# Kernel tuning notes

Measured on AMD Instinct MI355X. Metric: run time of the kernel, lower is better.

The kernel has to match this reference:

```python
import jax, jax.numpy as jnp
import numpy as np


def setup_inputs() -> dict:
    key = jax.random.key(0)
    ks = jax.random.split(key, 8)
    B, N, C = 4, 2048, 1024
    H, hd, lr, R = 16, 64, 20, 200  # R = low_rank * rank_multi
    s = lambda k, shape, fan: jax.random.normal(k, shape, jnp.float32) / np.sqrt(fan)
    return {
        'x': jax.random.normal(ks[0], (B, N, C), jnp.float32),
        'qk_w': s(ks[1], (2 * C, C), C),
        'proj_w': s(ks[2], (C, C), C),
        'proj_b': jnp.zeros((C,), jnp.float32),
        'we': s(ks[3], (H, R, lr), R),
        'wr': s(ks[4], (H, R, lr), R),
        'cw_w': s(ks[5], (hd, 2 * lr), 2 * lr),
        'cw_b': jnp.zeros((hd,), jnp.float32),
    }


def _l2norm(v, eps=1e-12):
    # matches F.normalize(p=2, dim=-1): x / max(||x||, eps)
    n = jnp.sqrt(jnp.sum(v * v, axis=-1, keepdims=True))
    return v / jnp.maximum(n, eps)


def reference(x, qk_w, proj_w, proj_b, we, wr, cw_w, cw_b):
    B, N, C = x.shape
    H, R, lr = we.shape  # heads, subsample len, low_rank
    hd = C // H
    # qk projection -> q,k: [B,H,N,hd]
    qk = (x @ qk_w.T).reshape(B, N, 2, H, hd).transpose(2, 0, 3, 1, 4)
    q, k = qk[0], qk[1]
    # gen_weights: subsample N positions (embed_len > low_rank*rank_multi branch)
    idx = np.linspace(0, N - 1, R).astype(np.int64)  # static, trunc like torch
    xh = x.transpose(0, 2, 1).reshape(B, H, hd, N)[:, :, :, idx]  # [B,H,hd,R]
    we_b = jnp.einsum('bhdr,hre->bhde', xh, we)  # [B,H,hd,lr]
    wr_b = jnp.einsum('bhdr,hre->bhde', xh, wr)
    # feature map + low-rank scores
    q = _l2norm(q)
    k = _l2norm(k)
    escore = jnp.einsum('bhnd,bhde->bhne', q, we_b)  # [B,H,N,lr]
    rscore = jnp.einsum('bhnd,bhde->bhne', k, wr_b)
    score = jnp.concatenate([escore, rscore], axis=-1)  # [B,H,N,2lr]
    attn = score @ cw_w.T + cw_b  # [B,H,N,hd]
    attn = attn.transpose(0, 2, 1, 3).reshape(B, N, C)
    out = attn @ proj_w.T + proj_b  # dropout is identity at eval
    return out
```

## Files before the change

### kernel.cpp

```cpp
#include <hip/hip_runtime.h>
#include <hip/hip_bf16.h>

constexpr int B_  = 4;
constexpr int N_  = 2048;
constexpr int C_  = 1024;
constexpr int H_  = 16;
constexpr int HD  = 64;
constexpr int LR  = 20;
constexpr int RS  = 200;
constexpr int RP  = 224;

typedef __attribute__((ext_vector_type(8))) short bf16x8;
typedef __attribute__((ext_vector_type(4))) float f32x4;

__device__ __forceinline__ float b2f_raw(unsigned short u) {
    union { unsigned int i; float f; } v;
    v.i = ((unsigned int)u) << 16;
    return v.f;
}
__device__ __forceinline__ unsigned short f2b(float f) {
    __hip_bfloat16 h = __float2bfloat16(f);
    return *(unsigned short*)&h;
}
template <bool BF>
__device__ __forceinline__ float ldg(const void* p, size_t i) {
    if constexpr (BF) return b2f_raw(((const unsigned short*)p)[i]);
    else              return ((const float*)p)[i];
}

__device__ __forceinline__ void async_load16(const unsigned short* g, unsigned short* l) {
    __builtin_amdgcn_global_load_lds(
        (const __attribute__((address_space(1))) unsigned int*)(const void*)g,
        (__attribute__((address_space(3))) unsigned int*)(void*)l,
        16, 0, 0);
}

__global__ __launch_bounds__(256)
void detect_kernel(const unsigned int* __restrict__ x, int* __restrict__ flag) {
    const int t = threadIdx.x;
    int cnt = 0;
    for (int i = t; i < 1024; i += 256) {
        const unsigned int w = x[i];
        const unsigned int e = (w >> 7) & 0xFFu;
        cnt += (e >= 103u && e <= 140u) ? 1 : 0;
    }
    __shared__ int s[256];
    s[t] = cnt;
    __syncthreads();
    for (int off = 128; off > 0; off >>= 1) {
        if (t < off) s[t] += s[t + off];
        __syncthreads();
    }
    if (t == 0) *flag = (s[0] > 512) ? 1 : 0;
}

struct CvtArgs {
    const void* src[5];
    unsigned short* dst[5];
    int size[5];
};

template <bool BF>
__device__ void wec_body(const void* __restrict__ we_raw,
                         const void* __restrict__ wr_raw,
                         const void* __restrict__ cw_raw,
                         unsigned short* __restrict__ wect,
                         unsigned short* __restrict__ wrct) {
    const int o = blockIdx.x * 256 + threadIdx.x;
    if (o >= H_ * HD * RP) return;
    const int r    = o % RP;
    const int dout = (o / RP) % HD;
    const int h    = o / (RP * HD);
    float sq = 0.f, sk = 0.f;
    if (r < RS) {
        #pragma unroll
        for (int e = 0; e < LR; ++e) {
            const float cq = ldg<BF>(cw_raw, dout * 2 * LR + e);
            const float ck = ldg<BF>(cw_raw, dout * 2 * LR + LR + e);
            sq += ldg<BF>(we_raw, ((size_t)h * RS + r) * LR + e) * cq;
            sk += ldg<BF>(wr_raw, ((size_t)h * RS + r) * LR + e) * ck;
        }
    }
    wect[o] = f2b(sq);
    wrct[o] = f2b(sk);
}

template <bool BF>
__device__ void gather_body(const void* __restrict__ x_raw,
                            unsigned short* __restrict__ xh) {
    const int bh = blockIdx.x;
    if (bh >= B_ * H_) return;
    const int b = bh >> 4;
    const int h = bh & 15;
    for (int o = threadIdx.x; o < HD * RP; o += 256) {
        const int din = o & 63;
        const int r   = o >> 6;
        unsigned short v = 0;
        if (r < RS) {
            const int ir = (r * (N_ - 1)) / (RS - 1);
            const size_t idx = ((size_t)b * N_ + ir) * C_ + h * HD + din;
            if constexpr (BF) v = ((const unsigned short*)x_raw)[idx];
            else              v = f2b(((const float*)x_raw)[idx]);
        }
        xh[(size_t)bh * HD * RP + (size_t)din * RP + r] = v;
    }
}

__global__ __launch_bounds__(256)
void fused_prep_kernel(const int* __restrict__ flag, CvtArgs args,
                       const void* __restrict__ we_raw,
                       const void* __restrict__ wr_raw,
                       const void* __restrict__ cw_raw,
                       unsigned short* __restrict__ wect,
                       unsigned short* __restrict__ wrct,
                       unsigned short* __restrict__ xh) {
    const bool isbf = (*flag != 0);
    const int y = blockIdx.y;
    if (y < 5) {
        const int n4 = args.size[y] >> 2;
        const int stride = gridDim.x * blockDim.x;
        for (int i = blockIdx.x * blockDim.x + threadIdx.x; i < n4; i += stride) {
            ushort4 o;
            if (isbf) {
                o = ((const ushort4*)args.src[y])[i];
            } else {
                const float4 v = ((const float4*)args.src[y])[i];
                o.x = f2b(v.x); o.y = f2b(v.y); o.z = f2b(v.z); o.w = f2b(v.w);
            }
            ((ushort4*)args.dst[y])[i] = o;
        }
    } else if (y == 5) {
        if (isbf) wec_body<true>(we_raw, wr_raw, cw_raw, wect, wrct);
        else      wec_body<false>(we_raw, wr_raw, cw_raw, wect, wrct);
    } else {
        if (isbf) gather_body<true>(args.src[0], xh);
        else      gather_body<false>(args.src[0], xh);
    }
}

__global__ __launch_bounds__(64)
void collapse_kernel(const unsigned short* __restrict__ xh,
                     const unsigned short* __restrict__ wect,
                     const unsigned short* __restrict__ wrct,
                     unsigned short* __restrict__ we2t,
                     unsigned short* __restrict__ wr2t) {
    const int blk = blockIdx.x;
    const int bh  = blk >> 2;
    const int qk  = (blk >> 1) & 1;
    const int dh  = blk & 1;
    const int h   = bh & 15;
    const int lane = threadIdx.x;
    const int lq = lane >> 4;
    const int lm = lane & 15;

    const unsigned short* wsrc = (qk ? wrct : wect) + (size_t)h * HD * RP;
    const unsigned short* xsrc = xh + (size_t)bh * HD * RP;
    unsigned short* dst = (qk ? wr2t : we2t) + (size_t)bh * HD * HD;

    f32x4 acc[2][4];
    #pragma unroll
    for (int i = 0; i < 2; ++i)
        #pragma unroll
        for (int j = 0; j < 4; ++j) acc[i][j] = 0.f;

    for (int ks = 0; ks < RP / 32; ++ks) {
        bf16x8 a[2], bfr[4];
        #pragma unroll
        for (int rt = 0; rt < 2; ++rt)
            a[rt] = *(const bf16x8*)&wsrc[(size_t)(dh * 32 + rt * 16 + lm) * RP + ks * 32 + lq * 8];
        #pragma unroll
        for (int j = 0; j < 4; ++j)
            bfr[j] = *(const bf16x8*)&xsrc[(size_t)(j * 16 + lm) * RP + ks * 32 + lq * 8];
        #pragma unroll
        for (int rt = 0; rt < 2; ++rt)
            #pragma unroll
            for (int j = 0; j < 4; ++j)
                acc[rt][j] = __builtin_amdgcn_mfma_f32_16x16x32_bf16(
                    a[rt], bfr[j], acc[rt][j], 0, 0, 0);
    }

    #pragma unroll
    for (int rt = 0; rt < 2; ++rt)
        #pragma unroll
        for (int j = 0; j < 4; ++j)
            #pragma unroll
            for (int r = 0; r < 4; ++r) {
                const int dout = dh * 32 + rt * 16 + lq * 4 + r;
                const int din  = j * 16 + lm;
                dst[dout * HD + din] = f2b(acc[rt][j][r]);
            }
}

__global__ __launch_bounds__(256)
void gemm1_score_kernel(const unsigned short* __restrict__ xb,
                        const unsigned short* __restrict__ qkwb,
                        const unsigned short* __restrict__ we2t,
                        const unsigned short* __restrict__ wr2t,
                        const unsigned short* __restrict__ cwbb,
                        unsigned short* __restrict__ attn) {
    constexpr int QS = 72;
    __shared__ __align__(16) unsigned short pool[2 * 128 * QS];
    unsigned short* As0 = pool;
    unsigned short* As1 = pool + 4096;
    unsigned short* Bs0 = pool + 8192;
    unsigned short* Bs1 = pool + 12288;
    unsigned short* qn  = pool;
    unsigned short* kn  = pool + 128 * QS;

    const int t    = threadIdx.x;
    const int wave = t >> 6;
    const int lane = t & 63;
    const int h    = blockIdx.x;
    const int m0   = blockIdx.y * 128;
    const int K    = C_;

    const int srow = lane >> 2;
    const int scol = (lane & 3) * 8;
    const unsigned short* ga0 = xb + (size_t)(m0 + wave * 16 + srow) * K + scol;
    const unsigned short* ga1 = xb + (size_t)(m0 + (wave + 4) * 16 + srow) * K + scol;
    const unsigned short* gb0 = qkwb + (size_t)(h * HD + wave * 16 + srow) * K + scol;
    const unsigned short* gb1 = qkwb + (size_t)(C_ + h * HD + wave * 16 + srow) * K + scol;
    unsigned short* lAa = &As0[wave * 512];
    unsigned short* lAb = &As0[(wave + 4) * 512];
    unsigned short* lBa = &Bs0[wave * 512];
    unsigned short* lBb = &Bs0[(wave + 4) * 512];
    unsigned short* lAa1 = &As1[wave * 512];
    unsigned short* lAb1 = &As1[(wave + 4) * 512];
    unsigned short* lBa1 = &Bs1[wave * 512];
    unsigned short* lBb1 = &Bs1[(wave + 4) * 512];

    const int wr = (wave >> 1) * 64;
    const int wc = (wave & 1) * 64;
    const int lq = lane >> 4;
    const int lm = lane & 15;

    f32x4 acc[4][4];
    #pragma unroll
    for (int i = 0; i < 4; ++i)
        #pragma unroll
        for (int j = 0; j < 4; ++j) acc[i][j] = 0.f;

    for (int k0 = 0; k0 < K; k0 += 64) {
        async_load16(ga0, lAa);  async_load16(ga0 + 32, lAa1);
        async_load16(ga1, lAb);  async_load16(ga1 + 32, lAb1);
        async_load16(gb0, lBa);  async_load16(gb0 + 32, lBa1);
        async_load16(gb1, lBb);  async_load16(gb1 + 32, lBb1);
        ga0 += 64; ga1 += 64; gb0 += 64; gb1 += 64;
        __syncthreads();

        #pragma unroll
        for (int h2 = 0; h2 < 2; ++h2) {
            const unsigned short* As = h2 ? As1 : As0;
            const unsigned short* Bs = h2 ? Bs1 : Bs0;
            bf16x8 af[4], bfr[4];
            #pragma unroll
            for (int i = 0; i < 4; ++i)
                af[i] = *(const bf16x8*)&As[(wr + i * 16 + lm) * 32 + lq * 8];
            #pragma unroll
            for (int j = 0; j < 4; ++j)
                bfr[j] = *(const bf16x8*)&Bs[(wc + j * 16 + lm) * 32 + lq * 8];
            #pragma unroll
            for (int i = 0; i < 4; ++i)
                #pragma unroll
                for (int j = 0; j < 4; ++j)
                    acc[i][j] = __builtin_amdgcn_mfma_f32_16x16x32_bf16(
                        af[i], bfr[j], acc[i][j], 0, 0, 0);
        }
        __syncthreads();
    }

    unsigned short* dst = (wc == 0) ? qn : kn;
    #pragma unroll
    for (int i = 0; i < 4; ++i) {
        float inv[4];
        #pragma unroll
        for (int r = 0; r < 4; ++r) {
            float s = 0.f;
            #pragma unroll
            for (int j = 0; j < 4; ++j) s += acc[i][j][r] * acc[i][j][r];
            s += __shfl_xor(s, 1, 64);
            s += __shfl_xor(s, 2, 64);
            s += __shfl_xor(s, 4, 64);
            s += __shfl_xor(s, 8, 64);
            inv[r] = 1.f / fmaxf(sqrtf(s), 1e-12f);
        }
        #pragma unroll
        for (int j = 0; j < 4; ++j)
            #pragma unroll
            for (int r = 0; r < 4; ++r) {
                const int row = wr + i * 16 + lq * 4 + r;
                dst[row * QS + j * 16 + lm] = f2b(acc[i][j][r] * inv[r]);
            }
    }
    __syncthreads();

    const int b  = blockIdx.y >> 4;
    const int bh = b * H_ + h;
    const unsigned short* wq = we2t + (size_t)bh * HD * HD;
    const unsigned short* wk = wr2t + (size_t)bh * HD * HD;

    bf16x8 bq[2][4], bk[2][4];
    #pragma unroll
    for (int t2 = 0; t2 < 2; ++t2)
        #pragma unroll
        for (int j = 0; j < 4; ++j) {
            const int dout = j * 16 + lm;
            bq[t2][j] = *(const bf16x8*)&wq[dout * HD + t2 * 32 + lq * 8];
            bk[t2][j] = *(const bf16x8*)&wk[dout * HD + t2 * 32 + lq * 8];
        }

    f32x4 accS[2][4];
    #pragma unroll
    for (int rt = 0; rt < 2; ++rt)
        #pragma unroll
        for (int j = 0; j < 4; ++j) accS[rt][j] = 0.f;

    #pragma unroll
    for (int rt = 0; rt < 2; ++rt) {
        const int lr = wave * 32 + rt * 16 + lm;
        bf16x8 aq0 = *(const bf16x8*)&qn[lr * QS + lq * 8];
        bf16x8 aq1 = *(const bf16x8*)&qn[lr * QS + 32 + lq * 8];
        bf16x8 ak0 = *(const bf16x8*)&kn[lr * QS + lq * 8];
        bf16x8 ak1 = *(const bf16x8*)&kn[lr * QS + 32 + lq * 8];
        #pragma unroll
        for (int j = 0; j < 4; ++j) {
            accS[rt][j] = __builtin_amdgcn_mfma_f32_16x16x32_bf16(aq0, bq[0][j], accS[rt][j], 0, 0, 0);
            accS[rt][j] = __builtin_amdgcn_mfma_f32_16x16x32_bf16(aq1, bq[1][j], accS[rt][j], 0, 0, 0);
            accS[rt][j] = __builtin_amdgcn_mfma_f32_16x16x32_bf16(ak0, bk[0][j], accS[rt][j], 0, 0, 0);
            accS[rt][j] = __builtin_amdgcn_mfma_f32_16x16x32_bf16(ak1, bk[1][j], accS[rt][j], 0, 0, 0);
        }
    }

    #pragma unroll
    for (int rt = 0; rt < 2; ++rt)
        #pragma unroll
        for (int j = 0; j < 4; ++j) {
            const int dout = j * 16 + lm;
            const float bv = b2f_raw(cwbb[dout]);
            #pragma unroll
            for (int r = 0; r < 4; ++r) {
                const int row = m0 + wave * 32 + rt * 16 + lq * 4 + r;
                attn[(size_t)row * C_ + h * HD + dout] = f2b(accS[rt][j][r] + bv);
            }
        }
}

template <bool OBF>
__device__ void mfma_gemm_body64(const unsigned short* __restrict__ A,
                                 const unsigned short* __restrict__ W,
                                 const unsigned short* __restrict__ bias,
                                 void* __restrict__ out,
                                 int M, int N, int K) {
    __shared__ __align__(16) unsigned short As0[4096], As1[4096];
    __shared__ __align__(16) unsigned short Bs0[4096], Bs1[4096];

    const int t    = threadIdx.x;
    const int wave = t >> 6;
    const int lane = t & 63;
    const int m0   = blockIdx.y * 128;
    const int n0   = blockIdx.x * 128;

    const int srow = lane >> 2;
    const int scol = (lane & 3) * 8;
    const unsigned short* ga0 = A + (size_t)(m0 + wave * 16 + srow) * K + scol;
    const unsigned short* ga1 = A + (size_t)(m0 + (wave + 4) * 16 + srow) * K + scol;
    const unsigned short* gb0 = W + (size_t)(n0 + wave * 16 + srow) * K + scol;
    const unsigned short* gb1 = W + (size_t)(n0 + (wave + 4) * 16 + srow) * K + scol;
    unsigned short* lAa  = &As0[wave * 512];
    unsigned short* lAb  = &As0[(wave + 4) * 512];
    unsigned short* lBa  = &Bs0[wave * 512];
    unsigned short* lBb  = &Bs0[(wave + 4) * 512];
    unsigned short* lAa1 = &As1[wave * 512];
    unsigned short* lAb1 = &As1[(wave + 4) * 512];
    unsigned short* lBa1 = &Bs1[wave * 512];
    unsigned short* lBb1 = &Bs1[(wave + 4) * 512];

    const int wr = (wave >> 1) * 64;
    const int wc = (wave & 1) * 64;
    const int lq = lane >> 4;
    const int lm = lane & 15;

    f32x4 acc[4][4];
    #pragma unroll
    for (int i = 0; i < 4; ++i)
        #pragma unroll
        for (int j = 0; j < 4; ++j) acc[i][j] = 0.f;

    for (int k0 = 0; k0 < K; k0 += 64) {
        async_load16(ga0, lAa);  async_load16(ga0 + 32, lAa1);
        async_load16(ga1, lAb);  async_load16(ga1 + 32, lAb1);
        async_load16(gb0, lBa);  async_load16(gb0 + 32, lBa1);
        async_load16(gb1, lBb);  async_load16(gb1 + 32, lBb1);
        ga0 += 64; ga1 += 64; gb0 += 64; gb1 += 64;
        __syncthreads();

        #pragma unroll
        for (int h2 = 0; h2 < 2; ++h2) {
            const unsigned short* As = h2 ? As1 : As0;
            const unsigned short* Bs = h2 ? Bs1 : Bs0;
            bf16x8 af[4], bfr[4];
            #pragma unroll
            for (int i = 0; i < 4; ++i)
                af[i] = *(const bf16x8*)&As[(wr + i * 16 + lm) * 32 + lq * 8];
            #pragma unroll
            for (int j = 0; j < 4; ++j)
                bfr[j] = *(const bf16x8*)&Bs[(wc + j * 16 + lm) * 32 + lq * 8];
            #pragma unroll
            for (int i = 0; i < 4; ++i)
                #pragma unroll
                for (int j = 0; j < 4; ++j)
                    acc[i][j] = __builtin_amdgcn_mfma_f32_16x16x32_bf16(
                        af[i], bfr[j], acc[i][j], 0, 0, 0);
        }
        __syncthreads();
    }

    #pragma unroll
    for (int i = 0; i < 4; ++i) {
        #pragma unroll
        for (int j = 0; j < 4; ++j) {
            const int col = n0 + wc + j * 16 + lm;
            const float bv = b2f_raw(bias[col]);
            #pragma unroll
            for (int r = 0; r < 4; ++r) {
                const int row = m0 + wr + i * 16 + lq * 4 + r;
                const float v = acc[i][j][r] + bv;
                if constexpr (OBF)
                    ((__hip_bfloat16*)out)[(size_t)row * N + col] = __float2bfloat16(v);
                else
                    ((float*)out)[(size_t)row * N + col] = v;
            }
        }
    }
}

__global__ __launch_bounds__(256)
void gemm2_kernel(const int* __restrict__ flag,
                  const unsigned short* __restrict__ attn,
                  const unsigned short* __restrict__ pwb,
                  const unsigned short* __restrict__ pbb,
                  void* __restrict__ out) {
    if (*flag) mfma_gemm_body64<true>(attn, pwb, pbb, out, B_ * N_, C_, C_);
    else       mfma_gemm_body64<false>(attn, pwb, pbb, out, B_ * N_, C_, C_);
}

extern "C" void kernel_launch(void* const* d_in, const int* in_sizes, int n_in,
                              void* d_out, int out_size, void* d_ws, size_t ws_size,
                              hipStream_t stream) {
    (void)in_sizes; (void)n_in; (void)out_size; (void)ws_size;

    char* ws = (char*)d_ws;
    size_t off = 0;
    auto alloc = [&](size_t bytes) {
        char* p = ws + off;
        off += (bytes + 255) & ~(size_t)255;
        return p;
    };

    int* flag = (int*)alloc(16);
    unsigned short* xb    = (unsigned short*)alloc((size_t)B_ * N_ * C_ * 2);
    unsigned short* qkwb  = (unsigned short*)alloc((size_t)2 * C_ * C_ * 2);
    unsigned short* pwb   = (unsigned short*)alloc((size_t)C_ * C_ * 2);
    unsigned short* pbb   = (unsigned short*)alloc((size_t)C_ * 2);
    unsigned short* cwbb  = (unsigned short*)alloc((size_t)HD * 2);
    unsigned short* attn  = (unsigned short*)alloc((size_t)B_ * N_ * C_ * 2);
    unsigned short* we2t  = (unsigned short*)alloc((size_t)B_ * H_ * HD * HD * 2);
    unsigned short* wr2t  = (unsigned short*)alloc((size_t)B_ * H_ * HD * HD * 2);
    unsigned short* wect  = (unsigned short*)alloc((size_t)H_ * HD * RP * 2);
    unsigned short* wrct  = (unsigned short*)alloc((size_t)H_ * HD * RP * 2);
    unsigned short* xh    = (unsigned short*)alloc((size_t)B_ * H_ * HD * RP * 2);

    const int M = B_ * N_;

    detect_kernel<<<1, 256, 0, stream>>>((const unsigned int*)d_in[0], flag);

    CvtArgs ca;
    ca.src[0] = d_in[0]; ca.dst[0] = xb;   ca.size[0] = B_ * N_ * C_;
    ca.src[1] = d_in[1]; ca.dst[1] = qkwb; ca.size[1] = 2 * C_ * C_;
    ca.src[2] = d_in[2]; ca.dst[2] = pwb;  ca.size[2] = C_ * C_;
    ca.src[3] = d_in[3]; ca.dst[3] = pbb;  ca.size[3] = C_;
    ca.src[4] = d_in[7]; ca.dst[4] = cwbb; ca.size[4] = HD;
    fused_prep_kernel<<<dim3(2048, 7), 256, 0, stream>>>(
        flag, ca, d_in[4], d_in[5], d_in[6], wect, wrct, xh);

    collapse_kernel<<<B_ * H_ * 4, 64, 0, stream>>>(xh, wect, wrct, we2t, wr2t);

    gemm1_score_kernel<<<dim3(H_, M / 128), 256, 0, stream>>>(
        xb, qkwb, we2t, wr2t, cwbb, attn);

    gemm2_kernel<<<dim3(C_ / 128, M / 128), 256, 0, stream>>>(
        flag, attn, pwb, pbb, d_out);
}
```

Before: 208.5 us.

## Double-buffer GEMM K-loop with XOR-swizzled LDS and occupancy launch bounds

Both GEMM main loops now work in K-steps of 32 and ping-pong between two LDS buffers. The async global-to-LDS load for the next tile is issued before the MFMA compute on the current one, so there is one barrier per step instead of a load, barrier, compute, barrier sequence. The LDS column is XOR-swizzled by row on both the store and read sides to reduce bank conflicts on the fragment reads. Launch bounds now ask for 4 blocks per CU, which may limit registers for the 64 accumulators and risk spills.

```diff
diff --git a/kernel.cpp b/kernel.cpp
--- a/kernel.cpp
+++ b/kernel.cpp
@@ -191,7 +191,7 @@
             }
 }
 
-__global__ __launch_bounds__(256)
+__global__ __launch_bounds__(256, 4)
 void gemm1_score_kernel(const unsigned short* __restrict__ xb,
                         const unsigned short* __restrict__ qkwb,
                         const unsigned short* __restrict__ we2t,
@@ -215,24 +215,17 @@
     const int K    = C_;
 
     const int srow = lane >> 2;
-    const int scol = (lane & 3) * 8;
+    const int scol = ((lane & 3) ^ ((srow >> 1) & 3)) * 8;
     const unsigned short* ga0 = xb + (size_t)(m0 + wave * 16 + srow) * K + scol;
-    const unsigned short* ga1 = xb + (size_t)(m0 + (wave + 4) * 16 + srow) * K + scol;
+    const unsigned short* ga1 = ga0 + (size_t)64 * K;
     const unsigned short* gb0 = qkwb + (size_t)(h * HD + wave * 16 + srow) * K + scol;
-    const unsigned short* gb1 = qkwb + (size_t)(C_ + h * HD + wave * 16 + srow) * K + scol;
-    unsigned short* lAa = &As0[wave * 512];
-    unsigned short* lAb = &As0[(wave + 4) * 512];
-    unsigned short* lBa = &Bs0[wave * 512];
-    unsigned short* lBb = &Bs0[(wave + 4) * 512];
-    unsigned short* lAa1 = &As1[wave * 512];
-    unsigned short* lAb1 = &As1[(wave + 4) * 512];
-    unsigned short* lBa1 = &Bs1[wave * 512];
-    unsigned short* lBb1 = &Bs1[(wave + 4) * 512];
+    const unsigned short* gb1 = gb0 + (size_t)C_ * K;
 
     const int wr = (wave >> 1) * 64;
     const int wc = (wave & 1) * 64;
     const int lq = lane >> 4;
     const int lm = lane & 15;
+    const int cx = (lq ^ ((lm >> 1) & 3)) * 8;
 
     f32x4 acc[4][4];
     #pragma unroll
@@ -240,34 +233,45 @@
         #pragma unroll
         for (int j = 0; j < 4; ++j) acc[i][j] = 0.f;
 
-    for (int k0 = 0; k0 < K; k0 += 64) {
-        async_load16(ga0, lAa);  async_load16(ga0 + 32, lAa1);
-        async_load16(ga1, lAb);  async_load16(ga1 + 32, lAb1);
-        async_load16(gb0, lBa);  async_load16(gb0 + 32, lBa1);
-        async_load16(gb1, lBb);  async_load16(gb1 + 32, lBb1);
-        ga0 += 64; ga1 += 64; gb0 += 64; gb1 += 64;
+    auto stage = [&](unsigned short* dA, unsigned short* dB) {
+        async_load16(ga0, dA + wave * 512);
+        async_load16(ga1, dA + (wave + 4) * 512);
+        async_load16(gb0, dB + wave * 512);
+        async_load16(gb1, dB + (wave + 4) * 512);
+        ga0 += 32; ga1 += 32; gb0 += 32; gb1 += 32;
+    };
+    auto compute = [&](const unsigned short* As, const unsigned short* Bs) {
+        bf16x8 af[4], bfr[4];
+        #pragma unroll
+        for (int i = 0; i < 4; ++i)
+            af[i] = *(const bf16x8*)&As[(wr + i * 16 + lm) * 32 + cx];
+        #pragma unroll
+        for (int j = 0; j < 4; ++j)
+            bfr[j] = *(const bf16x8*)&Bs[(wc + j * 16 + lm) * 32 + cx];
+        #pragma unroll
+        for (int i = 0; i < 4; ++i)
+            #pragma unroll
+            for (int j = 0; j < 4; ++j)
+                acc[i][j] = __builtin_amdgcn_mfma_f32_16x16x32_bf16(
+                    af[i], bfr[j], acc[i][j], 0, 0, 0);
+    };
+
+    constexpr int NT = C_ / 32;
+    stage(As0, Bs0);
+    __syncthreads();
+    for (int kt = 0; kt < NT - 2; kt += 2) {
+        stage(As1, Bs1);
+        compute(As0, Bs0);
         __syncthreads();
-
-        #pragma unroll
-        for (int h2 = 0; h2 < 2; ++h2) {
-            const unsigned short* As = h2 ? As1 : As0;
-            const unsigned short* Bs = h2 ? Bs1 : Bs0;
-            bf16x8 af[4], bfr[4];
-            #pragma unroll
-            for (int i = 0; i < 4; ++i)
-                af[i] = *(const bf16x8*)&As[(wr + i * 16 + lm) * 32 + lq * 8];
-            #pragma unroll
-            for (int j = 0; j < 4; ++j)
-                bfr[j] = *(const bf16x8*)&Bs[(wc + j * 16 + lm) * 32 + lq * 8];
-            #pragma unroll
-            for (int i = 0; i < 4; ++i)
-                #pragma unroll
-                for (int j = 0; j < 4; ++j)
-                    acc[i][j] = __builtin_amdgcn_mfma_f32_16x16x32_bf16(
-                        af[i], bfr[j], acc[i][j], 0, 0, 0);
-        }
+        stage(As0, Bs0);
+        compute(As1, Bs1);
         __syncthreads();
     }
+    stage(As1, Bs1);
+    compute(As0, Bs0);
+    __syncthreads();
+    compute(As1, Bs1);
+    __syncthreads();
 
     unsigned short* dst = (wc == 0) ? qn : kn;
     #pragma unroll
@@ -346,7 +350,7 @@
 }
 
 template <bool OBF>
-__device__ void mfma_gemm_body64(const unsigned short* __restrict__ A,
+__device__ void mfma_gemm_body32(const unsigned short* __restrict__ A,
                                  const unsigned short* __restrict__ W,
                                  const unsigned short* __restrict__ bias,
                                  void* __restrict__ out,
@@ -361,24 +365,17 @@
     const int n0   = blockIdx.x * 128;
 
     const int srow = lane >> 2;
-    const int scol = (lane & 3) * 8;
+    const int scol = ((lane & 3) ^ ((srow >> 1) & 3)) * 8;
     const unsigned short* ga0 = A + (size_t)(m0 + wave * 16 + srow) * K + scol;
-    const unsigned short* ga1 = A + (size_t)(m0 + (wave + 4) * 16 + srow) * K + scol;
+    const unsigned short* ga1 = ga0 + (size_t)64 * K;
     const unsigned short* gb0 = W + (size_t)(n0 + wave * 16 + srow) * K + scol;
-    const unsigned short* gb1 = W + (size_t)(n0 + (wave + 4) * 16 + srow) * K + scol;
-    unsigned short* lAa  = &As0[wave * 512];
-    unsigned short* lAb  = &As0[(wave + 4) * 512];
-    unsigned short* lBa  = &Bs0[wave * 512];
-    unsigned short* lBb  = &Bs0[(wave + 4) * 512];
-    unsigned short* lAa1 = &As1[wave * 512];
-    unsigned short* lAb1 = &As1[(wave + 4) * 512];
-    unsigned short* lBa1 = &Bs1[wave * 512];
-    unsigned short* lBb1 = &Bs1[(wave + 4) * 512];
+    const unsigned short* gb1 = gb0 + (size_t)64 * K;
 
     const int wr = (wave >> 1) * 64;
     const int wc = (wave & 1) * 64;
     const int lq = lane >> 4;
     const int lm = lane & 15;
+    const int cx = (lq ^ ((lm >> 1) & 3)) * 8;
 
     f32x4 acc[4][4];
     #pragma unroll
@@ -386,34 +383,44 @@
         #pragma unroll
         for (int j = 0; j < 4; ++j) acc[i][j] = 0.f;
 
-    for (int k0 = 0; k0 < K; k0 += 64) {
-        async_load16(ga0, lAa);  async_load16(ga0 + 32, lAa1);
-        async_load16(ga1, lAb);  async_load16(ga1 + 32, lAb1);
-        async_load16(gb0, lBa);  async_load16(gb0 + 32, lBa1);
-        async_load16(gb1, lBb);  async_load16(gb1 + 32, lBb1);
-        ga0 += 64; ga1 += 64; gb0 += 64; gb1 += 64;
+    auto stage = [&](unsigned short* dA, unsigned short* dB) {
+        async_load16(ga0, dA + wave * 512);
+        async_load16(ga1, dA + (wave + 4) * 512);
+        async_load16(gb0, dB + wave * 512);
+        async_load16(gb1, dB + (wave + 4) * 512);
+        ga0 += 32; ga1 += 32; gb0 += 32; gb1 += 32;
+    };
+    auto compute = [&](const unsigned short* As, const unsigned short* Bs) {
+        bf16x8 af[4], bfr[4];
+        #pragma unroll
+        for (int i = 0; i < 4; ++i)
+            af[i] = *(const bf16x8*)&As[(wr + i * 16 + lm) * 32 + cx];
+        #pragma unroll
+        for (int j = 0; j < 4; ++j)
+            bfr[j] = *(const bf16x8*)&Bs[(wc + j * 16 + lm) * 32 + cx];
+        #pragma unroll
+        for (int i = 0; i < 4; ++i)
+            #pragma unroll
+            for (int j = 0; j < 4; ++j)
+                acc[i][j] = __builtin_amdgcn_mfma_f32_16x16x32_bf16(
+                    af[i], bfr[j], acc[i][j], 0, 0, 0);
+    };
+
+    const int NT = K / 32;
+    stage(As0, Bs0);
+    __syncthreads();
+    for (int kt = 0; kt < NT - 2; kt += 2) {
+        stage(As1, Bs1);
+        compute(As0, Bs0);
         __syncthreads();
-
-        #pragma unroll
-        for (int h2 = 0; h2 < 2; ++h2) {
-            const unsigned short* As = h2 ? As1 : As0;
-            const unsigned short* Bs = h2 ? Bs1 : Bs0;
-            bf16x8 af[4], bfr[4];
-            #pragma unroll
-            for (int i = 0; i < 4; ++i)
-                af[i] = *(const bf16x8*)&As[(wr + i * 16 + lm) * 32 + lq * 8];
-            #pragma unroll
-            for (int j = 0; j < 4; ++j)
-                bfr[j] = *(const bf16x8*)&Bs[(wc + j * 16 + lm) * 32 + lq * 8];
-            #pragma unroll
-            for (int i = 0; i < 4; ++i)
-                #pragma unroll
-                for (int j = 0; j < 4; ++j)
-                    acc[i][j] = __builtin_amdgcn_mfma_f32_16x16x32_bf16(
-                        af[i], bfr[j], acc[i][j], 0, 0, 0);
-        }
+        stage(As0, Bs0);
+        compute(As1, Bs1);
         __syncthreads();
     }
+    stage(As1, Bs1);
+    compute(As0, Bs0);
+    __syncthreads();
+    compute(As1, Bs1);
 
     #pragma unroll
     for (int i = 0; i < 4; ++i) {
@@ -434,14 +441,14 @@
     }
 }
 
-__global__ __launch_bounds__(256)
+__global__ __launch_bounds__(256, 4)
 void gemm2_kernel(const int* __restrict__ flag,
                   const unsigned short* __restrict__ attn,
                   const unsigned short* __restrict__ pwb,
                   const unsigned short* __restrict__ pbb,
                   void* __restrict__ out) {
-    if (*flag) mfma_gemm_body64<true>(attn, pwb, pbb, out, B_ * N_, C_, C_);
-    else       mfma_gemm_body64<false>(attn, pwb, pbb, out, B_ * N_, C_, C_);
+    if (*flag) mfma_gemm_body32<true>(attn, pwb, pbb, out, B_ * N_, C_, C_);
+    else       mfma_gemm_body32<false>(attn, pwb, pbb, out, B_ * N_, C_, C_);
 }
 
 extern "C" void kernel_launch(void* const* d_in, const int* in_sizes, int n_in,
```

Measured after the change: 209.1 us. No clear change (+0.3%).

## Double-buffer GEMM K-loop with XOR-swizzled LDS tiles and occupancy hints

Applied to the files above, without the earlier changes.

Both GEMM kernels now use two LDS buffers so the async global-to-LDS loads for the next K tile are issued while MFMAs run on the current tile, leaving one barrier per iteration instead of two. The LDS tile layout changes to 64-wide rows with an XOR swizzle on the 16-byte column units to avoid bank conflicts on fragment reads. Launch bounds request two blocks per CU. LDS use per block doubles to 64 KB, which may limit occupancy, and the second launch-bounds argument may constrain register allocation.

```diff
diff --git a/kernel.cpp b/kernel.cpp
--- a/kernel.cpp
+++ b/kernel.cpp
@@ -191,7 +191,7 @@
             }
 }
 
-__global__ __launch_bounds__(256)
+__global__ __launch_bounds__(256, 2)
 void gemm1_score_kernel(const unsigned short* __restrict__ xb,
                         const unsigned short* __restrict__ qkwb,
                         const unsigned short* __restrict__ we2t,
@@ -199,13 +199,11 @@
                         const unsigned short* __restrict__ cwbb,
                         unsigned short* __restrict__ attn) {
     constexpr int QS = 72;
-    __shared__ __align__(16) unsigned short pool[2 * 128 * QS];
-    unsigned short* As0 = pool;
-    unsigned short* As1 = pool + 4096;
-    unsigned short* Bs0 = pool + 8192;
-    unsigned short* Bs1 = pool + 12288;
-    unsigned short* qn  = pool;
-    unsigned short* kn  = pool + 128 * QS;
+    __shared__ __align__(16) unsigned short pool[32768];
+    unsigned short* const AsBase = pool;
+    unsigned short* const BsBase = pool + 16384;
+    unsigned short* qn = pool;
+    unsigned short* kn = pool + 128 * QS;
 
     const int t    = threadIdx.x;
     const int wave = t >> 6;
@@ -214,25 +212,19 @@
     const int m0   = blockIdx.y * 128;
     const int K    = C_;
 
-    const int srow = lane >> 2;
-    const int scol = (lane & 3) * 8;
-    const unsigned short* ga0 = xb + (size_t)(m0 + wave * 16 + srow) * K + scol;
-    const unsigned short* ga1 = xb + (size_t)(m0 + (wave + 4) * 16 + srow) * K + scol;
-    const unsigned short* gb0 = qkwb + (size_t)(h * HD + wave * 16 + srow) * K + scol;
-    const unsigned short* gb1 = qkwb + (size_t)(C_ + h * HD + wave * 16 + srow) * K + scol;
-    unsigned short* lAa = &As0[wave * 512];
-    unsigned short* lAb = &As0[(wave + 4) * 512];
-    unsigned short* lBa = &Bs0[wave * 512];
-    unsigned short* lBb = &Bs0[(wave + 4) * 512];
-    unsigned short* lAa1 = &As1[wave * 512];
-    unsigned short* lAb1 = &As1[(wave + 4) * 512];
-    unsigned short* lBa1 = &Bs1[wave * 512];
-    unsigned short* lBb1 = &Bs1[(wave + 4) * 512];
+    const int srow  = lane >> 3;
+    const int sunit = (lane & 7) ^ srow;
+    const unsigned short* gA = xb + (size_t)(m0 + wave * 32 + srow) * K + sunit * 8;
+    const int vb = wave * 32;
+    const size_t brow = (vb < 64) ? (size_t)(h * HD + vb)
+                                  : (size_t)(C_ + h * HD + (vb - 64));
+    const unsigned short* gB = qkwb + (brow + srow) * K + sunit * 8;
 
     const int wr = (wave >> 1) * 64;
     const int wc = (wave & 1) * 64;
     const int lq = lane >> 4;
     const int lm = lane & 15;
+    const int c0 = (lq ^ (lm & 7)) * 8;
 
     f32x4 acc[4][4];
     #pragma unroll
@@ -240,25 +232,29 @@
         #pragma unroll
         for (int j = 0; j < 4; ++j) acc[i][j] = 0.f;
 
-    for (int k0 = 0; k0 < K; k0 += 64) {
-        async_load16(ga0, lAa);  async_load16(ga0 + 32, lAa1);
-        async_load16(ga1, lAb);  async_load16(ga1 + 32, lAb1);
-        async_load16(gb0, lBa);  async_load16(gb0 + 32, lBa1);
-        async_load16(gb1, lBb);  async_load16(gb1 + 32, lBb1);
-        ga0 += 64; ga1 += 64; gb0 += 64; gb1 += 64;
-        __syncthreads();
-
-        #pragma unroll
-        for (int h2 = 0; h2 < 2; ++h2) {
-            const unsigned short* As = h2 ? As1 : As0;
-            const unsigned short* Bs = h2 ? Bs1 : Bs0;
+    auto stage = [&](int buf) {
+        unsigned short* dA = AsBase + buf * 8192 + wave * 2048;
+        unsigned short* dB = BsBase + buf * 8192 + wave * 2048;
+        #pragma unroll
+        for (int i = 0; i < 4; ++i) {
+            async_load16(gA + (size_t)i * 8 * K, dA + i * 512);
+            async_load16(gB + (size_t)i * 8 * K, dB + i * 512);
+        }
+        gA += 64; gB += 64;
+    };
+    auto compute = [&](int buf) {
+        const unsigned short* As = AsBase + buf * 8192;
+        const unsigned short* Bs = BsBase + buf * 8192;
+        #pragma unroll
+        for (int ks = 0; ks < 2; ++ks) {
+            const int cc = c0 ^ (ks * 32);
             bf16x8 af[4], bfr[4];
             #pragma unroll
             for (int i = 0; i < 4; ++i)
-                af[i] = *(const bf16x8*)&As[(wr + i * 16 + lm) * 32 + lq * 8];
+                af[i] = *(const bf16x8*)&As[(wr + i * 16 + lm) * 64 + cc];
             #pragma unroll
             for (int j = 0; j < 4; ++j)
-                bfr[j] = *(const bf16x8*)&Bs[(wc + j * 16 + lm) * 32 + lq * 8];
+                bfr[j] = *(const bf16x8*)&Bs[(wc + j * 16 + lm) * 64 + cc];
             #pragma unroll
             for (int i = 0; i < 4; ++i)
                 #pragma unroll
@@ -266,8 +262,18 @@
                     acc[i][j] = __builtin_amdgcn_mfma_f32_16x16x32_bf16(
                         af[i], bfr[j], acc[i][j], 0, 0, 0);
         }
+    };
+
+    constexpr int NTK = C_ / 64;
+    stage(0);
+    __syncthreads();
+    for (int kt = 0; kt < NTK - 1; ++kt) {
+        stage((kt + 1) & 1);
+        compute(kt & 1);
         __syncthreads();
     }
+    compute((NTK - 1) & 1);
+    __syncthreads();
 
     unsigned short* dst = (wc == 0) ? qn : kn;
     #pragma unroll
@@ -351,8 +357,8 @@
                                  const unsigned short* __restrict__ bias,
                                  void* __restrict__ out,
                                  int M, int N, int K) {
-    __shared__ __align__(16) unsigned short As0[4096], As1[4096];
-    __shared__ __align__(16) unsigned short Bs0[4096], Bs1[4096];
+    __shared__ __align__(16) unsigned short AsBase[16384];
+    __shared__ __align__(16) unsigned short BsBase[16384];
 
     const int t    = threadIdx.x;
     const int wave = t >> 6;
@@ -360,25 +366,16 @@
     const int m0   = blockIdx.y * 128;
     const int n0   = blockIdx.x * 128;
 
-    const int srow = lane >> 2;
-    const int scol = (lane & 3) * 8;
-    const unsigned short* ga0 = A + (size_t)(m0 + wave * 16 + srow) * K + scol;
-    const unsigned short* ga1 = A + (size_t)(m0 + (wave + 4) * 16 + srow) * K + scol;
-    const unsigned short* gb0 = W + (size_t)(n0 + wave * 16 + srow) * K + scol;
-    const unsigned short* gb1 = W + (size_t)(n0 + (wave + 4) * 16 + srow) * K + scol;
-    unsigned short* lAa  = &As0[wave * 512];
-    unsigned short* lAb  = &As0[(wave + 4) * 512];
-    unsigned short* lBa  = &Bs0[wave * 512];
-    unsigned short* lBb  = &Bs0[(wave + 4) * 512];
-    unsigned short* lAa1 = &As1[wave * 512];
-    unsigned short* lAb1 = &As1[(wave + 4) * 512];
-    unsigned short* lBa1 = &Bs1[wave * 512];
-    unsigned short* lBb1 = &Bs1[(wave + 4) * 512];
+    const int srow  = lane >> 3;
+    const int sunit = (lane & 7) ^ srow;
+    const unsigned short* gA = A + (size_t)(m0 + wave * 32 + srow) * K + sunit * 8;
+    const unsigned short* gB = W + (size_t)(n0 + wave * 32 + srow) * K + sunit * 8;
 
     const int wr = (wave >> 1) * 64;
     const int wc = (wave & 1) * 64;
     const int lq = lane >> 4;
     const int lm = lane & 15;
+    const int c0 = (lq ^ (lm & 7)) * 8;
 
     f32x4 acc[4][4];
     #pragma unroll
@@ -386,25 +383,29 @@
         #pragma unroll
         for (int j = 0; j < 4; ++j) acc[i][j] = 0.f;
 
-    for (int k0 = 0; k0 < K; k0 += 64) {
-        async_load16(ga0, lAa);  async_load16(ga0 + 32, lAa1);
-        async_load16(ga1, lAb);  async_load16(ga1 + 32, lAb1);
-        async_load16(gb0, lBa);  async_load16(gb0 + 32, lBa1);
-        async_load16(gb1, lBb);  async_load16(gb1 + 32, lBb1);
-        ga0 += 64; ga1 += 64; gb0 += 64; gb1 += 64;
-        __syncthreads();
-
-        #pragma unroll
-        for (int h2 = 0; h2 < 2; ++h2) {
-            const unsigned short* As = h2 ? As1 : As0;
-            const unsigned short* Bs = h2 ? Bs1 : Bs0;
+    auto stage = [&](int buf) {
+        unsigned short* dA = AsBase + buf * 8192 + wave * 2048;
+        unsigned short* dB = BsBase + buf * 8192 + wave * 2048;
+        #pragma unroll
+        for (int i = 0; i < 4; ++i) {
+            async_load16(gA + (size_t)i * 8 * K, dA + i * 512);
+            async_load16(gB + (size_t)i * 8 * K, dB + i * 512);
+        }
+        gA += 64; gB += 64;
+    };
+    auto compute = [&](int buf) {
+        const unsigned short* As = AsBase + buf * 8192;
+        const unsigned short* Bs = BsBase + buf * 8192;
+        #pragma unroll
+        for (int ks = 0; ks < 2; ++ks) {
+            const int cc = c0 ^ (ks * 32);
             bf16x8 af[4], bfr[4];
             #pragma unroll
             for (int i = 0; i < 4; ++i)
-                af[i] = *(const bf16x8*)&As[(wr + i * 16 + lm) * 32 + lq * 8];
+                af[i] = *(const bf16x8*)&As[(wr + i * 16 + lm) * 64 + cc];
             #pragma unroll
             for (int j = 0; j < 4; ++j)
-                bfr[j] = *(const bf16x8*)&Bs[(wc + j * 16 + lm) * 32 + lq * 8];
+                bfr[j] = *(const bf16x8*)&Bs[(wc + j * 16 + lm) * 64 + cc];
             #pragma unroll
             for (int i = 0; i < 4; ++i)
                 #pragma unroll
@@ -412,8 +413,17 @@
                     acc[i][j] = __builtin_amdgcn_mfma_f32_16x16x32_bf16(
                         af[i], bfr[j], acc[i][j], 0, 0, 0);
         }
+    };
+
+    const int NTK = K / 64;
+    stage(0);
+    __syncthreads();
+    for (int kt = 0; kt < NTK - 1; ++kt) {
+        stage((kt + 1) & 1);
+        compute(kt & 1);
         __syncthreads();
     }
+    compute((NTK - 1) & 1);
 
     #pragma unroll
     for (int i = 0; i < 4; ++i) {
@@ -434,7 +444,7 @@
     }
 }
 
-__global__ __launch_bounds__(256)
+__global__ __launch_bounds__(256, 2)
 void gemm2_kernel(const int* __restrict__ flag,
                   const unsigned short* __restrict__ attn,
                   const unsigned short* __restrict__ pwb,
```

Measured after the change: 220.1 us. 5.6% more time.
